# Kernel tuning notes

Measured on AMD Instinct MI355X. Metric: run time of the kernel, lower is better.

## Reference

```python
import jax, jax.numpy as jnp
import numpy as np

B, S, D_IN = 2, 2048, 2048
N_HEADS, N_KV, HEAD_DIM = 16, 4, 128
GROUP = N_HEADS // N_KV  # 4
SCALING = 256.0 ** -0.5  # query_pre_attn_scalar = 256
EPS = 1e-6


def rms_norm(x, scale):
    # RMSNorm over last dim (head_dim)
    var = jnp.mean(jnp.square(x), axis=-1, keepdims=True)
    return x * jax.lax.rsqrt(var + EPS) * scale


def apply_rope(x, cos, sin):
    # x: [b, h, s, d]; cos/sin: [s, d]
    d = x.shape[-1]
    x1, x2 = x[..., : d // 2], x[..., d // 2 :]
    rotated = jnp.concatenate([-x2, x1], axis=-1)
    return x * cos[None, None, :, :] + rotated * sin[None, None, :, :]


def setup_inputs() -> dict:
    key = jax.random.key(0)
    ks = jax.random.split(key, 6)
    x = jax.random.normal(ks[0], (B, S, D_IN), dtype=jnp.float32)
    Wq = jax.random.normal(ks[1], (D_IN, N_HEADS * HEAD_DIM), dtype=jnp.float32) * 0.02
    Wk = jax.random.normal(ks[2], (D_IN, N_KV * HEAD_DIM), dtype=jnp.float32) * 0.02
    Wv = jax.random.normal(ks[3], (D_IN, N_KV * HEAD_DIM), dtype=jnp.float32) * 0.02
    Wo = jax.random.normal(ks[4], (N_HEADS * HEAD_DIM, D_IN), dtype=jnp.float32) * 0.02
    q_scale = jnp.ones((HEAD_DIM,), dtype=jnp.float32)
    k_scale = jnp.ones((HEAD_DIM,), dtype=jnp.float32)
    # RoPE tables: angles repeated twice across head_dim
    inv_freq = 1.0 / (10000.0 ** (np.arange(0, HEAD_DIM, 2, dtype=np.float32) / HEAD_DIM))
    angles = np.arange(S, dtype=np.float32)[:, None] * inv_freq[None, :]  # [S, d/2]
    angles = np.concatenate([angles, angles], axis=-1)  # [S, d]
    cos = jnp.asarray(np.cos(angles), dtype=jnp.float32)
    sin = jnp.asarray(np.sin(angles), dtype=jnp.float32)
    # causal mask: True = masked (future positions)
    mask = jnp.triu(jnp.ones((S, S), dtype=bool), k=1)
    return {"x": x, "mask": mask, "cos": cos, "sin": sin,
            "Wq": Wq, "Wk": Wk, "Wv": Wv, "Wo": Wo,
            "q_scale": q_scale, "k_scale": k_scale}


def reference(x, mask, cos, sin, Wq, Wk, Wv, Wo, q_scale, k_scale):
    b, s, _ = x.shape
    q = (x @ Wq).reshape(b, s, N_HEADS, HEAD_DIM).transpose(0, 2, 1, 3)  # [b,h,s,d]
    k = (x @ Wk).reshape(b, s, N_KV, HEAD_DIM).transpose(0, 2, 1, 3)     # [b,g,s,d]
    v = (x @ Wv).reshape(b, s, N_KV, HEAD_DIM).transpose(0, 2, 1, 3)
    # qk-norm
    q = rms_norm(q, q_scale)
    k = rms_norm(k, k_scale)
    # RoPE
    q = apply_rope(q, cos, sin)
    k = apply_rope(k, cos, sin)
    # repeat KV across groups
    k = jnp.repeat(k, GROUP, axis=1)  # [b,h,s,d]
    v = jnp.repeat(v, GROUP, axis=1)
    q = q * SCALING
    scores = jnp.einsum('bhqd,bhkd->bhqk', q, k)
    scores = jnp.where(mask, -jnp.inf, scores)
    weights = jax.nn.softmax(scores, axis=-1)
    ctx = jnp.einsum('bhqk,bhkd->bhqd', weights, v)
    ctx = ctx.transpose(0, 2, 1, 3).reshape(b, s, N_HEADS * HEAD_DIM)
    return ctx @ Wo
```

## Files before the change

### kernel.cpp

```cpp
#include <hip/hip_runtime.h>
#include <hip/hip_bf16.h>


using u16 = unsigned short;
using u32 = unsigned int;

constexpr int Ss  = 2048;
constexpr int Hh  = 16;
constexpr int KVH = 4;

typedef __attribute__((ext_vector_type(8))) short bf16x8;
typedef __attribute__((ext_vector_type(4))) float f32x4;

__device__ inline float b2f(u16 v)  { return __uint_as_float(((u32)v) << 16); }
__device__ inline u16 f2bf(float x) {
  u32 u = __float_as_uint(x);
  return (u16)((u + 0x7fffu + ((u >> 16) & 1u)) >> 16);
}
__device__ inline u32 cvtpk(float lo, float hi) {
  u32 r;
  asm("v_cvt_pk_bf16_f32 %0, %1, %2" : "=v"(r) : "v"(lo), "v"(hi));
  return r;
}

typedef const __attribute__((address_space(1))) unsigned int gas_u32;
typedef __attribute__((address_space(3))) unsigned int las_u32;
__device__ inline void gl16(const void* g, void* l) {
  __builtin_amdgcn_global_load_lds((gas_u32*)g, (las_u32*)l, 16, 0, 0);
}

__global__ __launch_bounds__(256) void cvt_bf16(const float* __restrict__ in,
                                                u16* __restrict__ out, int n4) {
  int i = blockIdx.x * 256 + threadIdx.x;
  if (i < n4) {
    float4 f = reinterpret_cast<const float4*>(in)[i];
    ushort4 o;
    o.x = f2bf(f.x); o.y = f2bf(f.y); o.z = f2bf(f.z); o.w = f2bf(f.w);
    reinterpret_cast<ushort4*>(out)[i] = o;
  }
}

__global__ __launch_bounds__(256) void tcvt(const float* __restrict__ in,
                                            u16* __restrict__ out, int N, int K) {
  __shared__ u16 T[64][66];
  const int k0 = blockIdx.x * 64, n0 = blockIdx.y * 64;
  const int c = threadIdx.x & 63, rb = threadIdx.x >> 6;
#pragma unroll
  for (int p = 0; p < 16; p++) {
    int r = p * 4 + rb;
    T[c][r] = f2bf(in[(size_t)(k0 + r) * N + n0 + c]);
  }
  __syncthreads();
  const int c2 = threadIdx.x & 31, rb2 = threadIdx.x >> 5;
#pragma unroll
  for (int p = 0; p < 8; p++) {
    int nr = p * 8 + rb2;
    u32 v = *reinterpret_cast<const u32*>(&T[nr][c2 * 2]);
    *reinterpret_cast<u32*>(out + (size_t)(n0 + nr) * K + k0 + c2 * 2) = v;
  }
}

__global__ __launch_bounds__(256) void vtrans(const u16* __restrict__ kv,
                                              u16* __restrict__ vT) {
  __shared__ u16 T[64][66];
  const int s0 = blockIdx.x * 64, d0 = blockIdx.y * 64, z = blockIdx.z;
  const int b = z >> 2, kvh = z & 3;
  const int c = threadIdx.x & 63, rb = threadIdx.x >> 6;
#pragma unroll
  for (int p = 0; p < 16; p++) {
    int r = p * 4 + rb;
    T[c][r] = kv[(size_t)(b * Ss + s0 + r) * 1024 + 512 + kvh * 128 + d0 + c];
  }
  __syncthreads();
  const int c2 = threadIdx.x & 31, rb2 = threadIdx.x >> 5;
#pragma unroll
  for (int p = 0; p < 8; p++) {
    int dr = p * 8 + rb2;
    u32 v = *reinterpret_cast<const u32*>(&T[dr][c2 * 2]);
    *reinterpret_cast<u32*>(vT + ((size_t)z * 128 + d0 + dr) * Ss + s0 + c2 * 2) = v;
  }
}

template <int MODE>
__global__ __launch_bounds__(256, 2) void gemm128(const u16* __restrict__ A,
                                                  const u16* __restrict__ Bt,
                                                  void* __restrict__ C0,
                                                  u16* __restrict__ C1,
                                                  int K) {
  __shared__ u16 As[2][128 * 64];
  __shared__ u16 Bs[2][128 * 64];
  const int t = threadIdx.x;
  const int wid = t >> 6, lane = t & 63;
  const int lrow = lane & 15, quad = lane >> 4;
  const int wm = wid >> 1, wn = wid & 1;
  const int m0 = blockIdx.x * 128, n0 = blockIdx.y * 128;
  const int sw8 = (lrow & 7) << 3;

  const int srow = t >> 3;
  const int sco  = ((t & 7) ^ (srow & 7)) * 8;

  f32x4 acc[4][4];
#pragma unroll
  for (int i = 0; i < 4; i++)
#pragma unroll
    for (int j = 0; j < 4; j++) acc[i][j] = (f32x4)0.f;

#define STAGE(buf, k0)                                                     \
  {                                                                        \
    _Pragma("unroll") for (int p = 0; p < 4; p++) {                        \
      gl16(A + (size_t)(m0 + p * 32 + srow) * K + (k0) + sco,              \
           (char*)As[buf] + (p * 256 + t) * 16);                           \
      gl16(Bt + (size_t)(n0 + p * 32 + srow) * K + (k0) + sco,             \
           (char*)Bs[buf] + (p * 256 + t) * 16);                           \
    }                                                                      \
  }

  const int nk = K >> 6;
  STAGE(0, 0)
  STAGE(1, 64)
  asm volatile("s_waitcnt vmcnt(8)" ::: "memory");
  __builtin_amdgcn_s_barrier();
  __builtin_amdgcn_sched_barrier(0);

  for (int kt = 0; kt < nk; ++kt) {
    const int buf = kt & 1;
#pragma unroll
    for (int kc = 0; kc < 2; kc++) {
      bf16x8 af[4], bfr[4];
#pragma unroll
      for (int i = 0; i < 4; i++)
        af[i] = *reinterpret_cast<const bf16x8*>(
            &As[buf][(wm * 64 + i * 16 + lrow) * 64 + (((kc * 4 + quad) << 3) ^ sw8)]);
#pragma unroll
      for (int j = 0; j < 4; j++)
        bfr[j] = *reinterpret_cast<const bf16x8*>(
            &Bs[buf][(wn * 64 + j * 16 + lrow) * 64 + (((kc * 4 + quad) << 3) ^ sw8)]);
      __builtin_amdgcn_s_setprio(1);
#pragma unroll
      for (int i = 0; i < 4; i++)
#pragma unroll
        for (int j = 0; j < 4; j++)
          acc[i][j] =
              __builtin_amdgcn_mfma_f32_16x16x32_bf16(af[i], bfr[j], acc[i][j], 0, 0, 0);
      __builtin_amdgcn_s_setprio(0);
    }
    __builtin_amdgcn_sched_barrier(0);
    __builtin_amdgcn_s_barrier();
    __builtin_amdgcn_sched_barrier(0);
    if (kt + 2 < nk) {
      STAGE(buf, (kt + 2) * 64)
    }
    if (kt + 1 < nk) {
      if (kt + 2 < nk) {
        asm volatile("s_waitcnt vmcnt(8)" ::: "memory");
      } else {
        asm volatile("s_waitcnt vmcnt(0)" ::: "memory");
      }
      __builtin_amdgcn_s_barrier();
      __builtin_amdgcn_sched_barrier(0);
    }
  }
#undef STAGE

  if (MODE == 0) {
    u16* C;
    int stride, coff;
    if (n0 < 2048) { C = (u16*)C0; stride = 2048; coff = n0; }
    else           { C = C1;       stride = 1024; coff = n0 - 2048; }
#pragma unroll
    for (int i = 0; i < 4; i++)
#pragma unroll
      for (int j = 0; j < 4; j++)
#pragma unroll
        for (int r = 0; r < 4; r++) {
          int row = m0 + wm * 64 + i * 16 + quad * 4 + r;
          int col = coff + wn * 64 + j * 16 + lrow;
          C[(size_t)row * stride + col] = f2bf(acc[i][j][r]);
        }
  } else {
    float* C = (float*)C0;
#pragma unroll
    for (int i = 0; i < 4; i++)
#pragma unroll
      for (int j = 0; j < 4; j++)
#pragma unroll
        for (int r = 0; r < 4; r++) {
          int row = m0 + wm * 64 + i * 16 + quad * 4 + r;
          int col = n0 + wn * 64 + j * 16 + lrow;
          C[(size_t)row * 2048 + col] = acc[i][j][r];
        }
  }
}

__global__ __launch_bounds__(256) void rmsrope2(u16* __restrict__ qbuf,
                                                u16* __restrict__ kvb,
                                                const float* __restrict__ qsc,
                                                const float* __restrict__ ksc,
                                                const float* __restrict__ cosb,
                                                const float* __restrict__ sinb) {
  const int w = threadIdx.x >> 6, lane = threadIdx.x & 63;
  const int vi = blockIdx.x * 4 + w;
  const int tok = vi / 20, j = vi - tok * 20;
  const int s = tok & (Ss - 1);
  const bool isq = j < 16;
  u16* p = isq ? (qbuf + (size_t)tok * 2048 + j * 128)
               : (kvb + (size_t)tok * 1024 + (j - 16) * 128);
  const float* scale = isq ? qsc : ksc;
  const float mult = isq ? 0.0625f : 1.0f;

  u32* p32 = reinterpret_cast<u32*>(p);
  u32 v = p32[lane];
  float e0 = b2f((u16)(v & 0xffff)), e1 = b2f((u16)(v >> 16));
  float ss = e0 * e0 + e1 * e1;
#pragma unroll
  for (int off = 32; off > 0; off >>= 1) ss += __shfl_xor(ss, off);
  float rr = rsqrtf(ss * (1.0f / 128.0f) + 1e-6f);
  float2 sc = reinterpret_cast<const float2*>(scale)[lane];
  float x0 = e0 * rr * sc.x;
  float x1 = e1 * rr * sc.y;
  float px0 = __shfl_xor(x0, 32);
  float px1 = __shfl_xor(x1, 32);
  float2 c  = reinterpret_cast<const float2*>(cosb + s * 128)[lane];
  float2 sn = reinterpret_cast<const float2*>(sinb + s * 128)[lane];
  float sgn = (lane < 32) ? -1.0f : 1.0f;
  float o0 = (x0 * c.x + sgn * px0 * sn.x) * mult;
  float o1 = (x1 * c.y + sgn * px1 * sn.y) * mult;
  p32[lane] = cvtpk(o0, o1);
}

__global__ __launch_bounds__(128, 2) void attn_mfma(const u16* __restrict__ qb,
                                                    const u16* __restrict__ kv,
                                                    const u16* __restrict__ vT,
                                                    u16* __restrict__ ctx) {
  __shared__ u16 Ks[64 * 128];
  __shared__ u16 Ps[2][32 * 40];
  const int i = blockIdx.x;
  const int g8 = i & 7, s = i >> 3;
  const int r = s >> 5, pos = s & 31;
  const int qtile = (r & 1) ? pos : 31 - pos;
  const int kvh = g8 & 3, b = g8 >> 2;
  const int h = kvh * 4 + r;
  const int t = threadIdx.x, w = t >> 6, lane = t & 63;
  const int lrow = lane & 15, quad = lane >> 4;
  const int qw = qtile * 64 + w * 32;

  const u16* kbase = kv + (size_t)b * Ss * 1024 + kvh * 128;
  const u16* vbase = vT + (size_t)(b * KVH + kvh) * 128 * Ss;

  const int kr  = t >> 4;
  const int kco = ((t & 15) ^ (kr & 7)) * 8;
  const int sw8 = (lrow & 7) << 3;

  bf16x8 qf[2][4];
#pragma unroll
  for (int g = 0; g < 2; g++)
#pragma unroll
    for (int c = 0; c < 4; c++)
      qf[g][c] = *reinterpret_cast<const bf16x8*>(
          qb + ((size_t)(b * Ss + qw + g * 16 + lrow) * Hh + h) * 128 + c * 32 + quad * 8);

  f32x4 o[2][8];
#pragma unroll
  for (int g = 0; g < 2; g++)
#pragma unroll
    for (int n = 0; n < 8; n++) o[g][n] = (f32x4)0.f;
  float mx[2] = {-1e30f, -1e30f}, ls[2] = {0.f, 0.f};

  const int ntile = qtile + 1;
  for (int kt = 0; kt < ntile; kt++) {
    const int kb0 = kt * 64;
    __syncthreads();
#pragma unroll
    for (int p8 = 0; p8 < 8; p8++)
      gl16(kbase + (size_t)(kb0 + p8 * 8 + kr) * 1024 + kco,
           (char*)Ks + (p8 * 128 + t) * 16);
    __syncthreads();

    f32x4 st[2][4];
#pragma unroll
    for (int g = 0; g < 2; g++)
#pragma unroll
      for (int mt = 0; mt < 4; mt++) st[g][mt] = (f32x4)0.f;
#pragma unroll
    for (int c = 0; c < 4; c++) {
      bf16x8 kf[4];
#pragma unroll
      for (int mt = 0; mt < 4; mt++)
        kf[mt] = *reinterpret_cast<const bf16x8*>(
            &Ks[(mt * 16 + lrow) * 128 + ((((c * 4 + quad) << 3)) ^ sw8)]);
      __builtin_amdgcn_s_setprio(1);
#pragma unroll
      for (int mt = 0; mt < 4; mt++)
#pragma unroll
        for (int g = 0; g < 2; g++)
          st[g][mt] =
              __builtin_amdgcn_mfma_f32_16x16x32_bf16(kf[mt], qf[g][c], st[g][mt], 0, 0, 0);
      __builtin_amdgcn_s_setprio(0);
    }

    bf16x8 vfa[2][8];
#pragma unroll
    for (int c2 = 0; c2 < 2; c2++)
#pragma unroll
      for (int n = 0; n < 8; n++)
        vfa[c2][n] = *reinterpret_cast<const bf16x8*>(
            vbase + (size_t)(n * 16 + lrow) * Ss + kb0 + c2 * 32 + quad * 8);

    if (kb0 + 63 > qw) {
#pragma unroll
      for (int g = 0; g < 2; g++) {
        int qg = qw + g * 16 + lrow;
#pragma unroll
        for (int mt = 0; mt < 4; mt++) {
          int kg = kb0 + mt * 16 + quad * 4;
#pragma unroll
          for (int rr = 0; rr < 4; rr++)
            st[g][mt][rr] = (kg + rr > qg) ? -1e30f : st[g][mt][rr];
        }
      }
    }
    float tmv[2];
#pragma unroll
    for (int g = 0; g < 2; g++) {
      f32x4 m4;
#pragma unroll
      for (int rr = 0; rr < 4; rr++)
        m4[rr] = fmaxf(fmaxf(st[g][0][rr], st[g][1][rr]), fmaxf(st[g][2][rr], st[g][3][rr]));
      float tm = fmaxf(fmaxf(m4[0], m4[1]), fmaxf(m4[2], m4[3]));
      tm = fmaxf(tm, __shfl_xor(tm, 16));
      tm = fmaxf(tm, __shfl_xor(tm, 32));
      tmv[g] = tm;
    }
    if (__any((tmv[0] > mx[0] + 8.0f) || (tmv[1] > mx[1] + 8.0f))) {
#pragma unroll
      for (int g = 0; g < 2; g++) {
        float mn = fmaxf(mx[g], tmv[g]);
        float a = __expf(mx[g] - mn);
        mx[g] = mn;
        ls[g] *= a;
#pragma unroll
        for (int n = 0; n < 8; n++) o[g][n] *= a;
      }
    }
#pragma unroll
    for (int g = 0; g < 2; g++) {
      float tsum = 0.f;
#pragma unroll
      for (int mt = 0; mt < 4; mt++)
#pragma unroll
        for (int rr = 0; rr < 4; rr++) {
          float pv = __expf(st[g][mt][rr] - mx[g]);
          st[g][mt][rr] = pv;
          tsum += pv;
        }
      tsum += __shfl_xor(tsum, 16);
      tsum += __shfl_xor(tsum, 32);
      ls[g] += tsum;
    }
#pragma unroll
    for (int c2 = 0; c2 < 2; c2++) {
#pragma unroll
      for (int g = 0; g < 2; g++)
#pragma unroll
        for (int mh = 0; mh < 2; mh++) {
          const f32x4 sv = st[g][c2 * 2 + mh];
          uint2 pk;
          pk.x = cvtpk(sv[0], sv[1]);
          pk.y = cvtpk(sv[2], sv[3]);
          *reinterpret_cast<uint2*>(
              &Ps[w][(g * 16 + lrow) * 40 + mh * 16 + quad * 4]) = pk;
        }
      bf16x8 pfr[2];
#pragma unroll
      for (int g = 0; g < 2; g++)
        pfr[g] = *reinterpret_cast<const bf16x8*>(
            &Ps[w][(g * 16 + lrow) * 40 + quad * 8]);
      __builtin_amdgcn_s_setprio(1);
#pragma unroll
      for (int n = 0; n < 8; n++)
#pragma unroll
        for (int g = 0; g < 2; g++)
          o[g][n] = __builtin_amdgcn_mfma_f32_16x16x32_bf16(vfa[c2][n], pfr[g], o[g][n], 0, 0, 0);
      __builtin_amdgcn_s_setprio(0);
    }
  }

#pragma unroll
  for (int g = 0; g < 2; g++) {
    float linv = 1.0f / ls[g];
    u16* obase = ctx + ((size_t)(b * Ss + qw + g * 16 + lrow) * Hh + h) * 128 + quad * 4;
#pragma unroll
    for (int n = 0; n < 8; n++) {
      uint2 pk;
      pk.x = cvtpk(o[g][n][0] * linv, o[g][n][1] * linv);
      pk.y = cvtpk(o[g][n][2] * linv, o[g][n][3] * linv);
      *reinterpret_cast<uint2*>(obase + n * 16) = pk;
    }
  }
}

extern "C" void kernel_launch(void* const* d_in, const int* in_sizes, int n_in,
                              void* d_out, int out_size, void* d_ws, size_t ws_size,
                              hipStream_t stream) {
  const float* x    = (const float*)d_in[0];
  const float* cosb = (const float*)d_in[2];
  const float* sinb = (const float*)d_in[3];
  const float* Wq   = (const float*)d_in[4];
  const float* Wk   = (const float*)d_in[5];
  const float* Wv   = (const float*)d_in[6];
  const float* Wo   = (const float*)d_in[7];
  const float* qsc  = (const float*)d_in[8];
  const float* ksc  = (const float*)d_in[9];

  const int M = 2 * Ss;
  u16* xb   = (u16*)d_ws;
  u16* Wqkv = xb + (size_t)8388608;
  u16* qbuf = Wqkv + (size_t)6291456;
  u16* kvb  = qbuf + (size_t)8388608;
  u16* vTb  = xb;
  u16* WoT  = Wqkv;

  cvt_bf16<<<8192, 256, 0, stream>>>(x, xb, 2097152);

  tcvt<<<dim3(32, 32), 256, 0, stream>>>(Wq, Wqkv, 2048, 2048);
  tcvt<<<dim3(32, 8), 256, 0, stream>>>(Wk, Wqkv + (size_t)2048 * 2048, 512, 2048);
  tcvt<<<dim3(32, 8), 256, 0, stream>>>(Wv, Wqkv + (size_t)2560 * 2048, 512, 2048);

  gemm128<0><<<dim3(32, 24), 256, 0, stream>>>(xb, Wqkv, qbuf, kvb, 2048);

  rmsrope2<<<(M * 20) / 4, 256, 0, stream>>>(qbuf, kvb, qsc, ksc, cosb, sinb);

  vtrans<<<dim3(32, 2, 8), 256, 0, stream>>>(kvb, vTb);

  attn_mfma<<<dim3(1024), 128, 0, stream>>>(qbuf, kvb, vTb, qbuf );

  tcvt<<<dim3(32, 32), 256, 0, stream>>>(Wo, WoT, 2048, 2048);
  gemm128<1><<<dim3(32, 16), 256, 0, stream>>>(qbuf, WoT, d_out, nullptr, 2048);
}
```

Baseline: 350.3 us.

## Fuse QKV weight conversions, single-buffer GEMM, stage V through LDS in attention

Merges the three Wq/Wk/Wv transpose-convert launches into one kernel so there are fewer launches. Replaces the double-buffered, prefetching GEMM main loop with a simple single-buffer load-sync-compute loop and asks for 3 blocks per CU, trading latency hiding for occupancy. In attention, V tiles are now copied into LDS with async global-to-LDS loads next to K instead of being read directly from global memory into registers. The block-to-tile mapping is also reordered to balance causal work across heads. The GEMM loses copy/compute overlap, which is a risk.

New measurement: 319.3 us. 8.8% less time.

```diff
diff --git a/kernel.cpp b/kernel.cpp
--- a/kernel.cpp
+++ b/kernel.cpp
@@ -40,6 +40,34 @@
   }
 }
 
+__global__ __launch_bounds__(256) void tcvt3(const float* __restrict__ Wq,
+                                             const float* __restrict__ Wk,
+                                             const float* __restrict__ Wv,
+                                             u16* __restrict__ out) {
+  __shared__ u16 T[64][66];
+  const int y = blockIdx.y, k0 = blockIdx.x * 64;
+  const float* in;
+  u16* o;
+  int N, n0;
+  if (y < 32)      { in = Wq; o = out;                         N = 2048; n0 = y * 64; }
+  else if (y < 40) { in = Wk; o = out + (size_t)2048 * 2048;   N = 512;  n0 = (y - 32) * 64; }
+  else             { in = Wv; o = out + (size_t)2560 * 2048;   N = 512;  n0 = (y - 40) * 64; }
+  const int c = threadIdx.x & 63, rb = threadIdx.x >> 6;
+#pragma unroll
+  for (int p = 0; p < 16; p++) {
+    int r = p * 4 + rb;
+    T[c][r] = f2bf(in[(size_t)(k0 + r) * N + n0 + c]);
+  }
+  __syncthreads();
+  const int c2 = threadIdx.x & 31, rb2 = threadIdx.x >> 5;
+#pragma unroll
+  for (int p = 0; p < 8; p++) {
+    int nr = p * 8 + rb2;
+    u32 v = *reinterpret_cast<const u32*>(&T[nr][c2 * 2]);
+    *reinterpret_cast<u32*>(o + (size_t)(n0 + nr) * 2048 + k0 + c2 * 2) = v;
+  }
+}
+
 __global__ __launch_bounds__(256) void tcvt(const float* __restrict__ in,
                                             u16* __restrict__ out, int N, int K) {
   __shared__ u16 T[64][66];
@@ -82,13 +110,13 @@
 }
 
 template <int MODE>
-__global__ __launch_bounds__(256, 2) void gemm128(const u16* __restrict__ A,
+__global__ __launch_bounds__(256, 3) void gemm_bt(const u16* __restrict__ A,
                                                   const u16* __restrict__ Bt,
                                                   void* __restrict__ C0,
                                                   u16* __restrict__ C1,
                                                   int K) {
-  __shared__ u16 As[2][128 * 64];
-  __shared__ u16 Bs[2][128 * 64];
+  __shared__ u16 As[128 * 64];
+  __shared__ u16 Bs[128 * 64];
   const int t = threadIdx.x;
   const int wid = t >> 6, lane = t & 63;
   const int lrow = lane & 15, quad = lane >> 4;
@@ -105,62 +133,35 @@
 #pragma unroll
     for (int j = 0; j < 4; j++) acc[i][j] = (f32x4)0.f;
 
-#define STAGE(buf, k0)                                                     \
-  {                                                                        \
-    _Pragma("unroll") for (int p = 0; p < 4; p++) {                        \
-      gl16(A + (size_t)(m0 + p * 32 + srow) * K + (k0) + sco,              \
-           (char*)As[buf] + (p * 256 + t) * 16);                           \
-      gl16(Bt + (size_t)(n0 + p * 32 + srow) * K + (k0) + sco,             \
-           (char*)Bs[buf] + (p * 256 + t) * 16);                           \
-    }                                                                      \
-  }
-
-  const int nk = K >> 6;
-  STAGE(0, 0)
-  STAGE(1, 64)
-  asm volatile("s_waitcnt vmcnt(8)" ::: "memory");
-  __builtin_amdgcn_s_barrier();
-  __builtin_amdgcn_sched_barrier(0);
-
-  for (int kt = 0; kt < nk; ++kt) {
-    const int buf = kt & 1;
+  for (int k0 = 0; k0 < K; k0 += 64) {
+    __syncthreads();
+#pragma unroll
+    for (int p = 0; p < 4; p++) {
+      gl16(A + (size_t)(m0 + p * 32 + srow) * K + k0 + sco,
+           (char*)As + (p * 256 + t) * 16);
+      gl16(Bt + (size_t)(n0 + p * 32 + srow) * K + k0 + sco,
+           (char*)Bs + (p * 256 + t) * 16);
+    }
+    __syncthreads();
 #pragma unroll
     for (int kc = 0; kc < 2; kc++) {
       bf16x8 af[4], bfr[4];
 #pragma unroll
       for (int i = 0; i < 4; i++)
         af[i] = *reinterpret_cast<const bf16x8*>(
-            &As[buf][(wm * 64 + i * 16 + lrow) * 64 + (((kc * 4 + quad) << 3) ^ sw8)]);
+            &As[(wm * 64 + i * 16 + lrow) * 64 + (((kc * 4 + quad) << 3) ^ sw8)]);
 #pragma unroll
       for (int j = 0; j < 4; j++)
         bfr[j] = *reinterpret_cast<const bf16x8*>(
-            &Bs[buf][(wn * 64 + j * 16 + lrow) * 64 + (((kc * 4 + quad) << 3) ^ sw8)]);
-      __builtin_amdgcn_s_setprio(1);
+            &Bs[(wn * 64 + j * 16 + lrow) * 64 + (((kc * 4 + quad) << 3) ^ sw8)]);
 #pragma unroll
       for (int i = 0; i < 4; i++)
 #pragma unroll
         for (int j = 0; j < 4; j++)
           acc[i][j] =
               __builtin_amdgcn_mfma_f32_16x16x32_bf16(af[i], bfr[j], acc[i][j], 0, 0, 0);
-      __builtin_amdgcn_s_setprio(0);
-    }
-    __builtin_amdgcn_sched_barrier(0);
-    __builtin_amdgcn_s_barrier();
-    __builtin_amdgcn_sched_barrier(0);
-    if (kt + 2 < nk) {
-      STAGE(buf, (kt + 2) * 64)
-    }
-    if (kt + 1 < nk) {
-      if (kt + 2 < nk) {
-        asm volatile("s_waitcnt vmcnt(8)" ::: "memory");
-      } else {
-        asm volatile("s_waitcnt vmcnt(0)" ::: "memory");
-      }
-      __builtin_amdgcn_s_barrier();
-      __builtin_amdgcn_sched_barrier(0);
-    }
-  }
-#undef STAGE
+    }
+  }
 
   if (MODE == 0) {
     u16* C;
@@ -233,15 +234,15 @@
                                                     const u16* __restrict__ vT,
                                                     u16* __restrict__ ctx) {
   __shared__ u16 Ks[64 * 128];
+  __shared__ u16 Vs[128 * 64];
   __shared__ u16 Ps[2][32 * 40];
   const int i = blockIdx.x;
-  const int g8 = i & 7, s = i >> 3;
-  const int r = s >> 5, pos = s & 31;
-  const int qtile = (r & 1) ? pos : 31 - pos;
-  const int kvh = g8 & 3, b = g8 >> 2;
-  const int h = kvh * 4 + r;
+  const int kq = i >> 8, jj = i & 255, x = jj >> 5, hb = jj & 31;
+  const int qtile = (kq == 0) ? 31 - x : (kq == 1) ? x : (kq == 2) ? 23 - x : 8 + x;
+  const int h = hb & 15, b = hb >> 4;
   const int t = threadIdx.x, w = t >> 6, lane = t & 63;
   const int lrow = lane & 15, quad = lane >> 4;
+  const int kvh = h >> 2;
   const int qw = qtile * 64 + w * 32;
 
   const u16* kbase = kv + (size_t)b * Ss * 1024 + kvh * 128;
@@ -249,6 +250,8 @@
 
   const int kr  = t >> 4;
   const int kco = ((t & 15) ^ (kr & 7)) * 8;
+  const int vr  = t >> 3;
+  const int vco = ((t & 7) ^ (vr & 7)) * 8;
   const int sw8 = (lrow & 7) << 3;
 
   bf16x8 qf[2][4];
@@ -271,9 +274,12 @@
     const int kb0 = kt * 64;
     __syncthreads();
 #pragma unroll
-    for (int p8 = 0; p8 < 8; p8++)
+    for (int p8 = 0; p8 < 8; p8++) {
       gl16(kbase + (size_t)(kb0 + p8 * 8 + kr) * 1024 + kco,
            (char*)Ks + (p8 * 128 + t) * 16);
+      gl16(vbase + (size_t)(p8 * 16 + vr) * Ss + kb0 + vco,
+           (char*)Vs + (p8 * 128 + t) * 16);
+    }
     __syncthreads();
 
     f32x4 st[2][4];
@@ -297,15 +303,6 @@
               __builtin_amdgcn_mfma_f32_16x16x32_bf16(kf[mt], qf[g][c], st[g][mt], 0, 0, 0);
       __builtin_amdgcn_s_setprio(0);
     }
-
-    bf16x8 vfa[2][8];
-#pragma unroll
-    for (int c2 = 0; c2 < 2; c2++)
-#pragma unroll
-      for (int n = 0; n < 8; n++)
-        vfa[c2][n] = *reinterpret_cast<const bf16x8*>(
-            vbase + (size_t)(n * 16 + lrow) * Ss + kb0 + c2 * 32 + quad * 8);
-
     if (kb0 + 63 > qw) {
 #pragma unroll
       for (int g = 0; g < 2; g++) {
@@ -377,10 +374,13 @@
             &Ps[w][(g * 16 + lrow) * 40 + quad * 8]);
       __builtin_amdgcn_s_setprio(1);
 #pragma unroll
-      for (int n = 0; n < 8; n++)
+      for (int n = 0; n < 8; n++) {
+        bf16x8 vf = *reinterpret_cast<const bf16x8*>(
+            &Vs[(n * 16 + lrow) * 64 + ((((c2 * 4 + quad) << 3)) ^ sw8)]);
 #pragma unroll
         for (int g = 0; g < 2; g++)
-          o[g][n] = __builtin_amdgcn_mfma_f32_16x16x32_bf16(vfa[c2][n], pfr[g], o[g][n], 0, 0, 0);
+          o[g][n] = __builtin_amdgcn_mfma_f32_16x16x32_bf16(vf, pfr[g], o[g][n], 0, 0, 0);
+      }
       __builtin_amdgcn_s_setprio(0);
     }
   }
@@ -422,11 +422,9 @@
 
   cvt_bf16<<<8192, 256, 0, stream>>>(x, xb, 2097152);
 
-  tcvt<<<dim3(32, 32), 256, 0, stream>>>(Wq, Wqkv, 2048, 2048);
-  tcvt<<<dim3(32, 8), 256, 0, stream>>>(Wk, Wqkv + (size_t)2048 * 2048, 512, 2048);
-  tcvt<<<dim3(32, 8), 256, 0, stream>>>(Wv, Wqkv + (size_t)2560 * 2048, 512, 2048);
-
-  gemm128<0><<<dim3(32, 24), 256, 0, stream>>>(xb, Wqkv, qbuf, kvb, 2048);
+  tcvt3<<<dim3(32, 48), 256, 0, stream>>>(Wq, Wk, Wv, Wqkv);
+
+  gemm_bt<0><<<dim3(32, 24), 256, 0, stream>>>(xb, Wqkv, qbuf, kvb, 2048);
 
   rmsrope2<<<(M * 20) / 4, 256, 0, stream>>>(qbuf, kvb, qsc, ksc, cosb, sinb);
 
@@ -435,5 +433,5 @@
   attn_mfma<<<dim3(1024), 128, 0, stream>>>(qbuf, kvb, vTb, qbuf );
 
   tcvt<<<dim3(32, 32), 256, 0, stream>>>(Wo, WoT, 2048, 2048);
-  gemm128<1><<<dim3(32, 16), 256, 0, stream>>>(qbuf, WoT, d_out, nullptr, 2048);
-}
+  gemm_bt<1><<<dim3(32, 16), 256, 0, stream>>>(qbuf, WoT, d_out, nullptr, 2048);
+}
```
